# Performance work log

Measured on AMD Instinct MI355X. Metric: run time of the kernel, lower is better.

Reference implementation:

```python
import jax, jax.numpy as jnp
import numpy as np

N_NODES = 4_194_304
N_GRAPHS = 65_536

# Orthonormal (Frobenius) basis for symmetric traceless 3x3 matrices: the
# real l=2 components of 1o x 1o -> 2e (Clebsch-Gordan up to basis choice).
_s2 = 1.0 / np.sqrt(2.0)
_B = np.zeros((5, 3, 3), dtype=np.float32)
_B[0, 0, 1] = _B[0, 1, 0] = _s2            # xy
_B[1, 1, 2] = _B[1, 2, 1] = _s2            # yz
_B[2, 0, 2] = _B[2, 2, 0] = _s2            # xz
_B[3, 0, 0] = _s2; _B[3, 1, 1] = -_s2      # x^2 - y^2
_B[4, 0, 0] = _B[4, 1, 1] = -1.0 / np.sqrt(6.0); _B[4, 2, 2] = 2.0 / np.sqrt(6.0)
B_CG = jnp.asarray(_B)

INV_SQRT2 = 0.7071067811865476
INV_SQRT3 = 0.5773502691896258


def setup_inputs() -> dict:
    key = jax.random.key(0)
    k1, k2, k3, k4, k5, k6 = jax.random.split(key, 6)
    z = jax.random.randint(k1, (N_NODES,), 0, 100, dtype=jnp.int32)
    pos = jax.random.normal(k2, (N_NODES, 3), dtype=jnp.float32)
    batch = jnp.sort(jax.random.randint(k3, (N_NODES,), 0, N_GRAPHS, dtype=jnp.int32))
    # FullyConnectedTensorProduct weights: 5 paths, mul pattern (1,1,mul_out)
    # 0e*0e->2x0e (2) + 1o*1o->2x0e (2) + 0e*1o->2x1o (2) + 1o*0e->2x1o (2) + 1o*1o->1x2e (1) = 9
    w_tp = jax.random.normal(k4, (9,), dtype=jnp.float32)
    fc_w = jax.random.normal(k5, (1, 13), dtype=jnp.float32) / np.sqrt(13.0)
    fc_b = jax.random.normal(k6, (1,), dtype=jnp.float32) * 0.01
    return {"z": z, "pos": pos, "batch": batch, "w_tp": w_tp, "fc_w": fc_w, "fc_b": fc_b}


def reference(z, pos, batch, w_tp, fc_w, fc_b):
    s = z.astype(jnp.float32)                      # [N] scalar (0e) part
    v = pos                                        # [N,3] vector (1o) part
    wA, wB = w_tp[0:2], w_tp[2:4]                  # -> 2x0e paths
    wC, wD = w_tp[4:6], w_tp[6:8]                  # -> 2x1o paths
    wE = w_tp[8]                                   # -> 1x2e path

    # CG tensor product x (x) x -> 2x0e + 2x1o + 1x2e, path-normalized by 1/sqrt(#paths)
    ss = s * s                                     # 0e x 0e -> 0e
    dot = jnp.sum(v * v, axis=-1)                  # 1o . 1o -> 0e (CG = delta/sqrt3)
    out0 = (ss[:, None] * wA + (dot * INV_SQRT3)[:, None] * wB) * INV_SQRT2   # [N,2]
    sv = s[:, None] * v                            # 0e x 1o -> 1o
    out1 = (sv[:, None, :] * (wC + wD)[None, :, None]) * INV_SQRT2            # [N,2,3]
    quad = jnp.einsum('kij,ni,nj->nk', B_CG, v, v) # 1o x 1o -> 2e            # [N,5]
    out2 = wE * quad

    x = jnp.concatenate([out0, out1.reshape(-1, 6), out2], axis=-1)  # [N,13]
    x = jax.nn.relu(x)                             # (as in source: relu on all irreps)
    y = x @ fc_w.T + fc_b                          # [N,1] -> 1x0e
    y = jnp.tanh(y)                                # Gate on pure scalars = scalar act

    sums = jax.ops.segment_sum(y, batch, num_segments=N_GRAPHS)                # [G,1]
    counts = jax.ops.segment_sum(jnp.ones((batch.shape[0], 1), y.dtype), batch,
                                 num_segments=N_GRAPHS)
    return sums / jnp.maximum(counts, 1.0)
```

## Files before the change

### kernel.cpp

```cpp
#include <hip/hip_runtime.h>

static constexpr float INV_SQRT2 = 0.70710678118654752f;
static constexpr float INV_SQRT3 = 0.57735026918962576f;
static constexpr float SQRT2     = 1.41421356237309505f;
static constexpr float INV_SQRT6 = 0.40824829046386302f;

static constexpr int W_GRAPHS = 8;
static constexpr int B_GRAPHS = 32;

__device__ __forceinline__ float fast_tanh(float x) {
    const float e = __builtin_amdgcn_exp2f(x * 2.8853900817779268f);
    const float r = __builtin_amdgcn_rcpf(e + 1.0f);
    return fmaf(-2.0f, r, 1.0f);
}

__device__ __forceinline__ float gate_p(float k, float fw) { return k > 0.f ? k * fw : 0.f; }
__device__ __forceinline__ float gate_n(float k, float fw) { return k < 0.f ? k * fw : 0.f; }

__global__ __launch_bounds__(256) void e3nn_fused(
    const int*   __restrict__ z,
    const float* __restrict__ pos,
    const int*   __restrict__ batch,
    const float* __restrict__ w_tp,
    const float* __restrict__ fc_w,
    const float* __restrict__ fc_b,
    float*       __restrict__ out,
    int n, int n_graphs)
{
    const int tid  = threadIdx.x;
    const int wid  = tid >> 6;
    const int lane = tid & 63;
    const int bg0  = blockIdx.x * B_GRAPHS;
    if (bg0 >= n_graphs) return;

    __shared__ int sbnd[B_GRAPHS + 1];

    if (wid == 0) {
        const int tl     = (lane < B_GRAPHS) ? lane : B_GRAPHS;
        const int target = bg0 + tl;
        unsigned p2 = 1;
        while (p2 < (unsigned)n) p2 <<= 1;
        int bv = 0;
        for (unsigned step = p2 >> 1; step > 0; step >>= 1) {
            const unsigned cand = (unsigned)bv + step;
            if (cand <= (unsigned)n && batch[cand - 1] < target) bv = (int)cand;
        }
        if (lane <= B_GRAPHS) sbnd[lane] = bv;
    }
    __syncthreads();

    const float kA0 = w_tp[0] * INV_SQRT2;
    const float kA1 = w_tp[1] * INV_SQRT2;
    const float kB0 = w_tp[2] * (INV_SQRT3 * INV_SQRT2);
    const float kB1 = w_tp[3] * (INV_SQRT3 * INV_SQRT2);
    const float c0  = (w_tp[4] + w_tp[6]) * INV_SQRT2;
    const float c1  = (w_tp[5] + w_tp[7]) * INV_SQRT2;
    const float wE  = w_tp[8];
    const float fw0 = fc_w[0], fw1 = fc_w[1];
    const float fb  = fc_b[0];

    const float P0 = gate_p(c0, fc_w[2]) + gate_p(c1, fc_w[5]);
    const float N0 = gate_n(c0, fc_w[2]) + gate_n(c1, fc_w[5]);
    const float P1 = gate_p(c0, fc_w[3]) + gate_p(c1, fc_w[6]);
    const float N1 = gate_n(c0, fc_w[3]) + gate_n(c1, fc_w[6]);
    const float P2 = gate_p(c0, fc_w[4]) + gate_p(c1, fc_w[7]);
    const float N2 = gate_n(c0, fc_w[4]) + gate_n(c1, fc_w[7]);
    const float k8  = wE * SQRT2,     k11 = wE * INV_SQRT2, k12 = wE * INV_SQRT6;
    const float P8  = gate_p(k8,  fc_w[8]),  N8  = gate_n(k8,  fc_w[8]);
    const float P9  = gate_p(k8,  fc_w[9]),  N9  = gate_n(k8,  fc_w[9]);
    const float P10 = gate_p(k8,  fc_w[10]), N10 = gate_n(k8,  fc_w[10]);
    const float P11 = gate_p(k11, fc_w[11]), N11 = gate_n(k11, fc_w[11]);
    const float P12 = gate_p(k12, fc_w[12]), N12 = gate_n(k12, fc_w[12]);

    const int wb = wid * W_GRAPHS;
    const int B0 = sbnd[wb + 0], B1 = sbnd[wb + 1];
    const int B2 = sbnd[wb + 2], B3 = sbnd[wb + 3];
    const int B4 = sbnd[wb + 4], B5 = sbnd[wb + 5];
    const int B6 = sbnd[wb + 6], B7 = sbnd[wb + 7];
    const int B8 = sbnd[wb + 8];
    const int myb = sbnd[wb + ((lane < W_GRAPHS) ? lane : W_GRAPHS)];
    const int nbv = sbnd[wb + ((lane < W_GRAPHS) ? lane + 1 : W_GRAPHS)];

    float tot = 0.f, s1 = 0.f, s2 = 0.f, s3 = 0.f;
    float s4  = 0.f, s5 = 0.f, s6 = 0.f, s7 = 0.f;

    auto body = [&](int i, float sc, float v0, float v1, float v2, bool valid) {
        const float v00 = v0 * v0, v11 = v1 * v1, v22 = v2 * v2;
        const float ss  = sc * sc;
        const float dr  = v00 + v11 + v22;

        float acc = fb;
        const float x0 = fmaf(ss, kA0, dr * kB0);
        const float x1 = fmaf(ss, kA1, dr * kB1);
        acc = fmaf(fmaxf(x0, 0.f), fw0, acc);
        acc = fmaf(fmaxf(x1, 0.f), fw1, acc);

        const float sv0 = sc * v0, sv1 = sc * v1, sv2 = sc * v2;
        acc = fmaf(sv0, (sv0 > 0.f ? P0 : N0), acc);
        acc = fmaf(sv1, (sv1 > 0.f ? P1 : N1), acc);
        acc = fmaf(sv2, (sv2 > 0.f ? P2 : N2), acc);

        const float t8 = v0 * v1, t9 = v1 * v2, t10 = v0 * v2;
        acc = fmaf(t8,  (t8  > 0.f ? P8  : N8 ), acc);
        acc = fmaf(t9,  (t9  > 0.f ? P9  : N9 ), acc);
        acc = fmaf(t10, (t10 > 0.f ? P10 : N10), acc);

        const float t11 = v00 - v11;
        acc = fmaf(t11, (t11 > 0.f ? P11 : N11), acc);
        const float t12 = (v22 - v00) + (v22 - v11);
        acc = fmaf(t12, (t12 > 0.f ? P12 : N12), acc);

        float y = fast_tanh(acc);
        if (!valid) y = 0.f;

        tot += y;
        s1 += (i >= B1) ? y : 0.f;
        s2 += (i >= B2) ? y : 0.f;
        s3 += (i >= B3) ? y : 0.f;
        s4 += (i >= B4) ? y : 0.f;
        s5 += (i >= B5) ? y : 0.f;
        s6 += (i >= B6) ? y : 0.f;
        s7 += (i >= B7) ? y : 0.f;
    };

    const int T = (B8 - B0) >> 6;

    float sc = 0.f, v0 = 0.f, v1 = 0.f, v2 = 0.f;
    if (T > 0) {
        const int gi = B0 + lane;
        sc = (float)z[gi];
        v0 = pos[3 * gi]; v1 = pos[3 * gi + 1]; v2 = pos[3 * gi + 2];
    }

#pragma unroll 1
    for (int t = 0; t < T; ++t) {
        float nsc = 0.f, n0 = 0.f, n1 = 0.f, n2 = 0.f;
        if (t + 1 < T) {
            const int gj = B0 + ((t + 1) << 6) + lane;
            nsc = (float)z[gj];
            n0 = pos[3 * gj]; n1 = pos[3 * gj + 1]; n2 = pos[3 * gj + 2];
        }
        body(B0 + (t << 6) + lane, sc, v0, v1, v2, true);
        sc = nsc; v0 = n0; v1 = n1; v2 = n2;
    }

    {
        const int tb = B0 + (T << 6);
        if (tb < B8) {
            const int i = tb + lane;
            float tsc = 0.f, t0 = 0.f, t1 = 0.f, t2 = 0.f;
            if (i < B8) {
                tsc = (float)z[i];
                t0 = pos[3 * i]; t1 = pos[3 * i + 1]; t2 = pos[3 * i + 2];
            }
            body(i, tsc, t0, t1, t2, i < B8);
        }
    }

#pragma unroll
    for (int off = 32; off >= 1; off >>= 1) {
        tot += __shfl_xor(tot, off);
        s1  += __shfl_xor(s1,  off);
        s2  += __shfl_xor(s2,  off);
        s3  += __shfl_xor(s3,  off);
        s4  += __shfl_xor(s4,  off);
        s5  += __shfl_xor(s5,  off);
        s6  += __shfl_xor(s6,  off);
        s7  += __shfl_xor(s7,  off);
    }

    const float a0 = tot - s1, a1 = s1 - s2, a2 = s2 - s3, a3 = s3 - s4;
    const float a4 = s4 - s5,  a5 = s5 - s6, a6 = s6 - s7, a7 = s7;

    const int gw0 = bg0 + wid * W_GRAPHS;
    if (lane < W_GRAPHS && gw0 + lane < n_graphs) {
        float sel = (lane == 0) ? a0
                  : (lane == 1) ? a1
                  : (lane == 2) ? a2
                  : (lane == 3) ? a3
                  : (lane == 4) ? a4
                  : (lane == 5) ? a5
                  : (lane == 6) ? a6
                  :               a7;
        const float c = (float)(nbv - myb);
        out[gw0 + lane] = sel / fmaxf(c, 1.0f);
    }
}

extern "C" void kernel_launch(void* const* d_in, const int* in_sizes, int n_in,
                              void* d_out, int out_size, void* d_ws, size_t ws_size,
                              hipStream_t stream) {
    const int*   z     = (const int*)d_in[0];
    const float* pos   = (const float*)d_in[1];
    const int*   batch = (const int*)d_in[2];
    const float* w_tp  = (const float*)d_in[3];
    const float* fc_w  = (const float*)d_in[4];
    const float* fc_b  = (const float*)d_in[5];

    float* out = (float*)d_out;
    const int n        = in_sizes[0];
    const int n_graphs = out_size;

    const int blocks = (n_graphs + B_GRAPHS - 1) / B_GRAPHS;
    e3nn_fused<<<blocks, 256, 0, stream>>>(z, pos, batch, w_tp, fc_w, fc_b,
                                           out, n, n_graphs);
}
```

Before: 27.20 us.

## Narrow boundary binary search with expected-position window and unroll main loop by two

```diff
diff --git a/kernel.cpp b/kernel.cpp
--- a/kernel.cpp
+++ b/kernel.cpp
@@ -38,12 +38,24 @@
     if (wid == 0) {
         const int tl     = (lane < B_GRAPHS) ? lane : B_GRAPHS;
         const int target = bg0 + tl;
-        unsigned p2 = 1;
-        while (p2 < (unsigned)n) p2 <<= 1;
-        int bv = 0;
-        for (unsigned step = p2 >> 1; step > 0; step >>= 1) {
-            const unsigned cand = (unsigned)bv + step;
-            if (cand <= (unsigned)n && batch[cand - 1] < target) bv = (int)cand;
+        int lo0 = (target << 6) - 8192;
+        lo0 = lo0 < 0 ? 0 : (lo0 > n ? n : lo0);
+        int bv = lo0;
+        #pragma unroll 1
+        for (int step = 8192; step > 0; step >>= 1) {
+            const int cand = bv + step;
+            if (cand <= n && batch[cand - 1] < target) bv = cand;
+        }
+        const bool ok = (bv == 0 || batch[bv - 1] < target) &&
+                        (bv >= n || batch[bv] >= target);
+        if (!__all(ok)) {
+            unsigned p2 = 1;
+            while (p2 < (unsigned)n) p2 <<= 1;
+            bv = 0;
+            for (unsigned step = p2; step > 0; step >>= 1) {
+                const unsigned cand = (unsigned)bv + step;
+                if (cand <= (unsigned)n && batch[cand - 1] < target) bv = (int)cand;
+            }
         }
         if (lane <= B_GRAPHS) sbnd[lane] = bv;
     }
@@ -123,38 +135,38 @@
         s7 += (i >= B7) ? y : 0.f;
     };
 
-    const int T = (B8 - B0) >> 6;
-
-    float sc = 0.f, v0 = 0.f, v1 = 0.f, v2 = 0.f;
-    if (T > 0) {
-        const int gi = B0 + lane;
-        sc = (float)z[gi];
-        v0 = pos[3 * gi]; v1 = pos[3 * gi + 1]; v2 = pos[3 * gi + 2];
-    }
+    const int T    = (B8 - B0) >> 6;
+    const int endf = B0 + (T << 6);
+    int base = B0;
 
 #pragma unroll 1
-    for (int t = 0; t < T; ++t) {
-        float nsc = 0.f, n0 = 0.f, n1 = 0.f, n2 = 0.f;
-        if (t + 1 < T) {
-            const int gj = B0 + ((t + 1) << 6) + lane;
-            nsc = (float)z[gj];
-            n0 = pos[3 * gj]; n1 = pos[3 * gj + 1]; n2 = pos[3 * gj + 2];
+    for (; base + 128 <= endf; base += 128) {
+        const int iA = base + lane;
+        const int iB = iA + 64;
+        const float scA = (float)z[iA];
+        const float scB = (float)z[iB];
+        const float a0 = pos[3 * iA], a1 = pos[3 * iA + 1], a2 = pos[3 * iA + 2];
+        const float b0 = pos[3 * iB], b1 = pos[3 * iB + 1], b2 = pos[3 * iB + 2];
+        body(iA, scA, a0, a1, a2, true);
+        body(iB, scB, b0, b1, b2, true);
+    }
+
+    if (base < endf) {
+        const int i = base + lane;
+        const float sc = (float)z[i];
+        const float v0 = pos[3 * i], v1 = pos[3 * i + 1], v2 = pos[3 * i + 2];
+        body(i, sc, v0, v1, v2, true);
+        base += 64;
+    }
+
+    if (base < B8) {
+        const int i = base + lane;
+        float sc = 0.f, v0 = 0.f, v1 = 0.f, v2 = 0.f;
+        if (i < B8) {
+            sc = (float)z[i];
+            v0 = pos[3 * i]; v1 = pos[3 * i + 1]; v2 = pos[3 * i + 2];
         }
-        body(B0 + (t << 6) + lane, sc, v0, v1, v2, true);
-        sc = nsc; v0 = n0; v1 = n1; v2 = n2;
-    }
-
-    {
-        const int tb = B0 + (T << 6);
-        if (tb < B8) {
-            const int i = tb + lane;
-            float tsc = 0.f, t0 = 0.f, t1 = 0.f, t2 = 0.f;
-            if (i < B8) {
-                tsc = (float)z[i];
-                t0 = pos[3 * i]; t1 = pos[3 * i + 1]; t2 = pos[3 * i + 2];
-            }
-            body(i, tsc, t0, t1, t2, i < B8);
-        }
+        body(i, sc, v0, v1, v2, i < B8);
     }
 
 #pragma unroll
```

New measurement: 27.86 us. +2.5%, slower.
